# Optimization experiments

Hardware: AMD Instinct MI355X
Metric: run time of the kernel (lower is better)

## Reference

```python
import jax, jax.numpy as jnp
import numpy as np

B, T, C = 2, 2048, 2048
N_HEAD, N_KV_HEAD, HEAD_DIM = 16, 4, 128
N_REP = N_HEAD // N_KV_HEAD
EPS = 1e-05


def setup_inputs() -> dict:
    key = jax.random.key(0)
    ks = jax.random.split(key, 8)
    # rope freqs as cos/sin of theta_t,i = t / 10000^(2i/d)
    inv_freq = 1.0 / (10000.0 ** (np.arange(0, HEAD_DIM, 2, dtype=np.float32) / HEAD_DIM))
    ang = np.arange(T, dtype=np.float32)[:, None] * inv_freq[None, :]  # [T, HEAD_DIM//2]
    scale = 0.02
    return {
        "x": jax.random.normal(ks[0], (B, T, C), jnp.float32),
        "freqs_cos": jnp.asarray(np.cos(ang)),
        "freqs_sin": jnp.asarray(np.sin(ang)),
        "wq": jax.random.normal(ks[1], (C, N_HEAD * HEAD_DIM), jnp.float32) * scale,
        "wk": jax.random.normal(ks[2], (C, N_KV_HEAD * HEAD_DIM), jnp.float32) * scale,
        "wv": jax.random.normal(ks[3], (C, N_KV_HEAD * HEAD_DIM), jnp.float32) * scale,
        "wo": jax.random.normal(ks[4], (N_HEAD * HEAD_DIM, C), jnp.float32) * scale,
        "q_norm_w": jnp.ones((HEAD_DIM,), jnp.float32),
        "k_norm_w": jnp.ones((HEAD_DIM,), jnp.float32),
    }


def _rmsnorm(x, w):
    var = jnp.mean(jnp.square(x), axis=-1, keepdims=True)
    return x * jax.lax.rsqrt(var + EPS) * w


def _rope(x, cos, sin):
    # x: [B, T, H, D]; interpret last dim as interleaved (real, imag) pairs
    xr = x[..., 0::2]
    xi = x[..., 1::2]
    c = cos[None, :, None, :]
    s = sin[None, :, None, :]
    out_r = xr * c - xi * s
    out_i = xr * s + xi * c
    return jnp.stack([out_r, out_i], axis=-1).reshape(x.shape)


def reference(x, freqs_cos, freqs_sin, wq, wk, wv, wo, q_norm_w, k_norm_w):
    # QKV projections
    xq = (x @ wq).reshape(B, T, N_HEAD, HEAD_DIM)
    xk = (x @ wk).reshape(B, T, N_KV_HEAD, HEAD_DIM)
    xv = (x @ wv).reshape(B, T, N_KV_HEAD, HEAD_DIM)
    # optional q/k RMSNorm (use_qk_norm=True)
    xq = _rmsnorm(xq, q_norm_w)
    xk = _rmsnorm(xk, k_norm_w)
    # RoPE
    xq = _rope(xq, freqs_cos, freqs_sin)
    xk = _rope(xk, freqs_cos, freqs_sin)
    # GQA expand: each kv head repeated N_REP times contiguously
    xk = jnp.repeat(xk, N_REP, axis=2)  # [B, T, N_HEAD, D]
    xv = jnp.repeat(xv, N_REP, axis=2)
    # causal SDPA
    scores = jnp.einsum("bthd,bshd->bhts", xq, xk) / jnp.sqrt(jnp.float32(HEAD_DIM))
    causal = jnp.tril(jnp.ones((T, T), bool))
    scores = jnp.where(causal[None, None], scores, jnp.float32(-1e30))
    attn = jax.nn.softmax(scores, axis=-1)
    y = jnp.einsum("bhts,bshd->bthd", attn, xv).reshape(B, T, N_HEAD * HEAD_DIM)
    return y @ wo
```

## Files before the change

### kernel.cpp

```cpp
#include <hip/hip_runtime.h>
#include <hip/hip_bf16.h>

using u16 = unsigned short;
using u32 = unsigned int;

typedef short bf16x8 __attribute__((ext_vector_type(8)));
typedef float f32x4 __attribute__((ext_vector_type(4)));

#define AS1 __attribute__((address_space(1)))
#define AS3 __attribute__((address_space(3)))

__device__ __forceinline__ void gll16(const void* g, void* l) {
  __builtin_amdgcn_global_load_lds((const AS1 u32*)g, (AS3 u32*)l, 16, 0, 0);
}

__device__ __forceinline__ u16 f2bf(float x) {
  u32 u = __builtin_bit_cast(u32, x);
  u32 r = (u + 0x7fffu + ((u >> 16) & 1u)) >> 16;
  return (u16)r;
}
__device__ __forceinline__ u32 pk2(float lo, float hi) {
  return (u32)f2bf(lo) | ((u32)f2bf(hi) << 16);
}
__device__ __forceinline__ u16 f2bf_fast(float x) {
  __hip_bfloat16 h = __float2bfloat16(x);
  return __builtin_bit_cast(u16, h);
}

__device__ __forceinline__ void trans64(const float* __restrict__ in, u16* __restrict__ out,
                                        int R, int Cc, int bx, int by, float (*tl)[65]) {
  int c0 = bx * 64, r0 = by * 64, tid = threadIdx.x;
#pragma unroll
  for (int i = 0; i < 16; i++) {
    int idx = i * 256 + tid; int tr = idx >> 6, tc = idx & 63;
    tl[tr][tc] = in[(size_t)(r0 + tr) * Cc + c0 + tc];
  }
  __syncthreads();
#pragma unroll
  for (int i = 0; i < 16; i++) {
    int idx = i * 256 + tid; int tr = idx >> 6, tc = idx & 63;
    out[(size_t)(c0 + tr) * R + r0 + tc] = f2bf(tl[tc][tr]);
  }
}

__global__ void k_prep(const float* __restrict__ x, u16* __restrict__ xb,
                       const float* __restrict__ wq, u16* __restrict__ wqt,
                       const float* __restrict__ wk, const float* __restrict__ wv,
                       u16* __restrict__ wkvt,
                       const float* __restrict__ wo, u16* __restrict__ wot,
                       const float* __restrict__ fc, const float* __restrict__ fs,
                       float2* __restrict__ fcs) {
  __shared__ float tl[64][65];
  int gid = blockIdx.x;
  if (gid < 4096) {
    int i = gid * 256 + threadIdx.x;
    const float4* p = (const float4*)(x + (size_t)i * 8);
    float4 a = p[0], b = p[1];
    uint4 o;
    o.x = pk2(a.x, a.y); o.y = pk2(a.z, a.w);
    o.z = pk2(b.x, b.y); o.w = pk2(b.z, b.w);
    *(uint4*)(xb + (size_t)i * 8) = o;
  } else if (gid < 5120) {
    int t = gid - 4096; trans64(wq, wqt, 2048, 2048, t & 31, t >> 5, tl);
  } else if (gid < 5376) {
    int t = gid - 5120; trans64(wk, wkvt, 2048, 512, t & 7, t >> 3, tl);
  } else if (gid < 5632) {
    int t = gid - 5376; trans64(wv, wkvt + 512 * 2048, 2048, 512, t & 7, t >> 3, tl);
  } else if (gid < 6656) {
    int t = gid - 5632; trans64(wo, wot, 2048, 2048, t & 31, t >> 5, tl);
  } else {
    int base = (gid - 6656) * 2048 + threadIdx.x * 8;
#pragma unroll
    for (int j = 0; j < 8; j++) {
      int idx = base + j;
      fcs[idx] = make_float2(fc[idx], fs[idx]);
    }
  }
}

__global__ __launch_bounds__(512, 2) void k_gemm_qkv(
    const u16* __restrict__ A, const u16* __restrict__ BT0, const u16* __restrict__ BT1,
    u16* __restrict__ Qout, u16* __restrict__ Kout, u16* __restrict__ Vout,
    const float* __restrict__ nwq, const float* __restrict__ nwk,
    const float2* __restrict__ fcs) {
  __shared__ char lds[131072];
  const int K = 2048;
  int tid = threadIdx.x, w = tid >> 6, l = tid & 63, lg = l >> 4, ll = l & 15;
  int wr = w >> 2, wc = w & 3;
  int lid = blockIdx.y * 24 + blockIdx.x;
  int xcd = lid & 7, r = lid >> 3;
  int colg = xcd & 1, rowg = xcd >> 1;
  int bxt = colg * 12 + r % 12;
  int bm0 = (rowg * 8 + r / 12) * 128;
  bool qpath = (bxt < 16);
  const u16* BT = qpath ? BT0 : BT1;
  int bn0 = qpath ? bxt * 128 : (bxt - 16) * 128;

  auto stage = [&](int si, int kt) {
    char* Sb = lds + si * 32768;
    int k0 = kt * 64;
#pragma unroll
    for (int i = 0; i < 2; i++) {
      int base = i * 512 + (w << 6);
      int c = base + l;
      int row = c >> 3, kc = (c & 7) ^ (row & 7);
      gll16(A + (size_t)(bm0 + row) * K + k0 + kc * 8, Sb + base * 16);
      gll16(BT + (size_t)(bn0 + row) * K + k0 + kc * 8, Sb + 16384 + base * 16);
    }
  };

  f32x4 acc[4][2] = {};
  stage(0, 0); stage(1, 1); stage(2, 2);
  asm volatile("s_waitcnt vmcnt(8)" ::: "memory");
  __builtin_amdgcn_s_barrier();
  __builtin_amdgcn_sched_barrier(0);

  for (int kt = 0; kt < 32; ++kt) {
    int cs = kt & 3;
    if (kt + 3 < 32) stage((kt + 3) & 3, kt + 3);
    char* As = lds + cs * 32768;
    char* Bs = As + 16384;
    __builtin_amdgcn_s_setprio(1);
#pragma unroll
    for (int ks = 0; ks < 2; ks++) {
      bf16x8 af[4], bf[2];
#pragma unroll
      for (int m = 0; m < 4; m++) {
        int row = 64 * wr + 16 * m + ll;
        af[m] = *(const bf16x8*)(As + row * 128 + (((lg + 4 * ks) ^ (row & 7)) << 4));
      }
#pragma unroll
      for (int n = 0; n < 2; n++) {
        int row = 32 * wc + 16 * n + ll;
        bf[n] = *(const bf16x8*)(Bs + row * 128 + (((lg + 4 * ks) ^ (row & 7)) << 4));
      }
#pragma unroll
      for (int m = 0; m < 4; m++)
#pragma unroll
        for (int n = 0; n < 2; n++)
          acc[m][n] = __builtin_amdgcn_mfma_f32_16x16x32_bf16(af[m], bf[n], acc[m][n], 0, 0, 0);
    }
    __builtin_amdgcn_s_setprio(0);
    if (kt <= 28) {
      asm volatile("s_waitcnt vmcnt(8)" ::: "memory");
    } else if (kt == 29) {
      asm volatile("s_waitcnt vmcnt(4)" ::: "memory");
    } else {
      asm volatile("s_waitcnt vmcnt(0)" ::: "memory");
    }
    __builtin_amdgcn_s_barrier();
    __builtin_amdgcn_sched_barrier(0);
  }

  if (qpath || bn0 < 512) {
    const float* nw = qpath ? nwq : nwk;
    u16* O = qpath ? Qout : Kout;
    int ostride = qpath ? 2048 : 512;
    float outscale = qpath ? 0.12751744843f : 1.0f;
    float* ssum = (float*)lds;
    float ps[4][4];
#pragma unroll
    for (int m = 0; m < 4; m++)
#pragma unroll
      for (int r2 = 0; r2 < 4; r2++) {
        float p = 0.f;
#pragma unroll
        for (int n = 0; n < 2; n++) p += acc[m][n][r2] * acc[m][n][r2];
#pragma unroll
        for (int msk = 1; msk < 16; msk <<= 1) p += __shfl_xor(p, msk);
        ps[m][r2] = p;
      }
    if (ll == 0) {
#pragma unroll
      for (int m = 0; m < 4; m++)
#pragma unroll
        for (int r2 = 0; r2 < 4; r2++)
          ssum[wr * 256 + (16 * m + 4 * lg + r2) * 4 + wc] = ps[m][r2];
    }
    __syncthreads();
    float rs[4][4];
#pragma unroll
    for (int m = 0; m < 4; m++)
#pragma unroll
      for (int r2 = 0; r2 < 4; r2++) {
        int rowl = 16 * m + 4 * lg + r2;
        const float* sp = ssum + wr * 256 + rowl * 4;
        float tot = sp[0] + sp[1] + sp[2] + sp[3];
        rs[m][r2] = rsqrtf(tot * (1.0f / 128.0f) + 1e-5f) * outscale;
      }
#pragma unroll
    for (int m = 0; m < 4; m++)
#pragma unroll
      for (int n = 0; n < 2; n++) {
        int col = bn0 + 32 * wc + 16 * n + ll;
        int d = col & 127;
        float wgt = nw[d];
        int i = d >> 1;
#pragma unroll
        for (int r2 = 0; r2 < 4; r2++) {
          int row = bm0 + 64 * wr + 16 * m + 4 * lg + r2;
          int t = row & 2047;
          float y = acc[m][n][r2] * rs[m][r2] * wgt;
          float p = __shfl_xor(y, 1);
          float2 cs2 = fcs[t * 64 + i];
          float o = (ll & 1) ? (p * cs2.y + y * cs2.x) : (y * cs2.x - p * cs2.y);
          O[(size_t)row * ostride + col] = f2bf(o);
        }
      }
  } else {
    int b = bm0 >> 11, t0g = bm0 & 2047;
    int kvh = (bn0 - 512) >> 7;
    int bk = b * 4 + kvh;
#pragma unroll
    for (int m = 0; m < 4; m++)
#pragma unroll
      for (int n = 0; n < 2; n++) {
        int d = 32 * wc + 16 * n + ll;
        int tloc = 64 * wr + 16 * m + 4 * lg;
        u32 w0 = pk2(acc[m][n][0], acc[m][n][1]);
        u32 w1 = pk2(acc[m][n][2], acc[m][n][3]);
        int byte = (d * 256 + tloc * 2) ^ ((d & 7) << 4);
        *(uint2*)(lds + byte) = make_uint2(w0, w1);
      }
    __syncthreads();
    int tc = tid & 15, dbase = tid >> 4;
#pragma unroll
    for (int pass = 0; pass < 4; pass++) {
      int d = dbase + pass * 32;
      int byte = (d * 256 + tc * 16) ^ ((d & 7) << 4);
      uint4 v = *(const uint4*)(lds + byte);
      *(uint4*)(Vout + ((size_t)(bk * 128 + d)) * 2048 + t0g + tc * 8) = v;
    }
  }
}

__global__ __launch_bounds__(512, 2) void k_gemm_o(
    const u16* __restrict__ A, const u16* __restrict__ BT, float* __restrict__ C) {
  __shared__ char lds[131072];
  const int K = 2048;
  int tid = threadIdx.x, w = tid >> 6, l = tid & 63, lg = l >> 4, ll = l & 15;
  int wr = w >> 2, wc = w & 3;
  int lid = blockIdx.y * 16 + blockIdx.x;
  int xcd = lid & 7, r = lid >> 3;
  int colg = xcd & 1, rowg = xcd >> 1;
  int bxt = colg * 8 + r % 8;
  int bm0 = (rowg * 8 + r / 8) * 128;
  int bn0 = bxt * 128;

  auto stage = [&](int si, int kt) {
    char* Sb = lds + si * 32768;
    int k0 = kt * 64;
#pragma unroll
    for (int i = 0; i < 2; i++) {
      int base = i * 512 + (w << 6);
      int c = base + l;
      int row = c >> 3, kc = (c & 7) ^ (row & 7);
      gll16(A + (size_t)(bm0 + row) * K + k0 + kc * 8, Sb + base * 16);
      gll16(BT + (size_t)(bn0 + row) * K + k0 + kc * 8, Sb + 16384 + base * 16);
    }
  };

  f32x4 acc[4][2] = {};
  stage(0, 0); stage(1, 1); stage(2, 2);
  asm volatile("s_waitcnt vmcnt(8)" ::: "memory");
  __builtin_amdgcn_s_barrier();
  __builtin_amdgcn_sched_barrier(0);

  for (int kt = 0; kt < 32; ++kt) {
    int cs = kt & 3;
    if (kt + 3 < 32) stage((kt + 3) & 3, kt + 3);
    char* As = lds + cs * 32768;
    char* Bs = As + 16384;
    __builtin_amdgcn_s_setprio(1);
#pragma unroll
    for (int ks = 0; ks < 2; ks++) {
      bf16x8 af[4], bf[2];
#pragma unroll
      for (int m = 0; m < 4; m++) {
        int row = 64 * wr + 16 * m + ll;
        af[m] = *(const bf16x8*)(As + row * 128 + (((lg + 4 * ks) ^ (row & 7)) << 4));
      }
#pragma unroll
      for (int n = 0; n < 2; n++) {
        int row = 32 * wc + 16 * n + ll;
        bf[n] = *(const bf16x8*)(Bs + row * 128 + (((lg + 4 * ks) ^ (row & 7)) << 4));
      }
#pragma unroll
      for (int m = 0; m < 4; m++)
#pragma unroll
        for (int n = 0; n < 2; n++)
          acc[m][n] = __builtin_amdgcn_mfma_f32_16x16x32_bf16(af[m], bf[n], acc[m][n], 0, 0, 0);
    }
    __builtin_amdgcn_s_setprio(0);
    if (kt <= 28) {
      asm volatile("s_waitcnt vmcnt(8)" ::: "memory");
    } else if (kt == 29) {
      asm volatile("s_waitcnt vmcnt(4)" ::: "memory");
    } else {
      asm volatile("s_waitcnt vmcnt(0)" ::: "memory");
    }
    __builtin_amdgcn_s_barrier();
    __builtin_amdgcn_sched_barrier(0);
  }

#pragma unroll
  for (int m = 0; m < 4; m++)
#pragma unroll
    for (int n = 0; n < 2; n++) {
      int row = bm0 + 64 * wr + 16 * m + 4 * lg;
      int col = bn0 + 32 * wc + 16 * n + ll;
      float* cp = C + (size_t)row * 2048 + col;
#pragma unroll
      for (int r2 = 0; r2 < 4; r2++) cp[(size_t)r2 * 2048] = acc[m][n][r2];
    }
}

__global__ __launch_bounds__(256, 4) void k_attn(
    const u16* __restrict__ Q, const u16* __restrict__ Kb,
    const u16* __restrict__ Vt, u16* __restrict__ Y) {
  __shared__ char lds[73728];
  char* Ps = lds + 65536;
  int tid = threadIdx.x, w = tid >> 6, l = tid & 63, lg = l >> 4, ll = l & 15;
  int fid = blockIdx.x;
  int g = fid & 7, rank = fid >> 3;
  int b = g >> 2, kvh = g & 3;
  int h = kvh * 4 + (rank & 3);
  int pairId = rank >> 2;
  const u16* Kbase = Kb + ((size_t)b * 2048) * 512 + kvh * 128;
  const u16* Vbase = Vt + ((size_t)(b * 4 + kvh) * 128) * 2048;

  const bf16x8 vones = {(short)0x3F80, (short)0x3F80, (short)0x3F80, (short)0x3F80,
                        (short)0x3F80, (short)0x3F80, (short)0x3F80, (short)0x3F80};

#pragma unroll 1
  for (int qi = 0; qi < 2; qi++) {
    int qb = qi ? (31 - pairId) : pairId;
    int q0 = qb * 64;
    bf16x8 qf[4];
    {
      int qrow = b * 2048 + q0 + 16 * w + ll;
      const u16* qp = Q + (size_t)qrow * 2048 + h * 128;
#pragma unroll
      for (int ks = 0; ks < 4; ks++) qf[ks] = *(const bf16x8*)(qp + ks * 32 + lg * 8);
    }
    f32x4 o[8] = {};
    f32x4 lacc = {};

    auto stage = [&](int bi, int k0) {
      char* Kd = lds + (bi ? 32768 : 0);
      char* Vd = lds + (bi ? 49152 : 16384);
#pragma unroll
      for (int i = 0; i < 4; i++) {
        int c = i * 256 + tid;
        int dst = (i * 256 + (w << 6)) * 16;
        int krow = c >> 4, ksrc = (c & 15) ^ (krow & 7);
        gll16(Kbase + (size_t)(k0 + krow) * 512 + ksrc * 8, Kd + dst);
        int vd = c >> 3, vsrc = (c & 7) ^ (vd & 7);
        gll16(Vbase + (size_t)vd * 2048 + k0 + vsrc * 8, Vd + dst);
      }
    };

    stage(0, 0);
    asm volatile("s_waitcnt vmcnt(0)" ::: "memory");
    __syncthreads();

    int cur = 0;
    for (int it = 0; it <= qb; ++it) {
      if (it < qb) stage(cur ^ 1, (it + 1) * 64);
      char* Ks = lds + (cur ? 32768 : 0);
      char* Vs = lds + (cur ? 49152 : 16384);
      f32x4 s[4] = {};
      __builtin_amdgcn_s_setprio(1);
#pragma unroll
      for (int ks = 0; ks < 4; ks++) {
#pragma unroll
        for (int n = 0; n < 4; n++) {
          int row = 16 * n + ll;
          bf16x8 kf = *(const bf16x8*)(Ks + ((row * 256 + (lg + 4 * ks) * 16) ^ ((row & 7) << 4)));
          s[n] = __builtin_amdgcn_mfma_f32_16x16x32_bf16(qf[ks], kf, s[n], 0, 0, 0);
        }
      }
      __builtin_amdgcn_s_setprio(0);
      if (it == qb) {
        int k0 = it * 64;
#pragma unroll
        for (int n = 0; n < 4; n++) {
          int kk = k0 + 16 * n + ll;
#pragma unroll
          for (int r = 0; r < 4; r++) {
            int qq = q0 + 16 * w + 4 * lg + r;
            if (kk > qq) s[n][r] = -1e30f;
          }
        }
      }
#pragma unroll
      for (int r = 0; r < 4; r++) {
        int prow = 4 * lg + r;
#pragma unroll
        for (int n = 0; n < 4; n++) {
          float e = exp2f(s[n][r]);
          int byte = (w << 11) + ((prow * 128 + (16 * n + ll) * 2) ^ ((prow & 7) << 4));
          *(u16*)(Ps + byte) = f2bf_fast(e);
        }
      }
      __builtin_amdgcn_s_setprio(1);
#pragma unroll
      for (int ks = 0; ks < 2; ks++) {
        bf16x8 pf = *(const bf16x8*)(Ps + (w << 11) + ((ll * 128 + (lg + 4 * ks) * 16) ^ ((ll & 7) << 4)));
        lacc = __builtin_amdgcn_mfma_f32_16x16x32_bf16(pf, vones, lacc, 0, 0, 0);
#pragma unroll
        for (int n = 0; n < 8; n++) {
          int row = 16 * n + ll;
          bf16x8 vf = *(const bf16x8*)(Vs + ((row * 128 + (lg + 4 * ks) * 16) ^ ((row & 7) << 4)));
          o[n] = __builtin_amdgcn_mfma_f32_16x16x32_bf16(pf, vf, o[n], 0, 0, 0);
        }
      }
      __builtin_amdgcn_s_setprio(0);
      asm volatile("s_waitcnt vmcnt(0)" ::: "memory");
      __syncthreads();
      cur ^= 1;
    }
    float rl[4];
#pragma unroll
    for (int r = 0; r < 4; r++) rl[r] = 1.0f / lacc[r];
#pragma unroll
    for (int n = 0; n < 8; n++) {
      int col = h * 128 + 16 * n + ll;
#pragma unroll
      for (int r = 0; r < 4; r++) {
        int trow = b * 2048 + q0 + 16 * w + 4 * lg + r;
        Y[(size_t)trow * 2048 + col] = f2bf_fast(o[n][r] * rl[r]);
      }
    }
  }
  (void)Vbase;
}

extern "C" void kernel_launch(void* const* d_in, const int* in_sizes, int n_in,
                              void* d_out, int out_size, void* d_ws, size_t ws_size,
                              hipStream_t stream) {
  const float* x   = (const float*)d_in[0];
  const float* fc  = (const float*)d_in[1];
  const float* fs  = (const float*)d_in[2];
  const float* wq  = (const float*)d_in[3];
  const float* wk  = (const float*)d_in[4];
  const float* wv  = (const float*)d_in[5];
  const float* wo  = (const float*)d_in[6];
  const float* qnw = (const float*)d_in[7];
  const float* knw = (const float*)d_in[8];
  float* out = (float*)d_out;

  const size_t MB = 1ull << 20;
  char* ws = (char*)d_ws;
  u16*    xb   = (u16*)(ws);
  u16*    wqt  = (u16*)(ws + 16 * MB);
  u16*    wkvt = (u16*)(ws + 24 * MB);
  u16*    wot  = (u16*)(ws + 28 * MB);
  u16*    Qb   = (u16*)(ws + 36 * MB);
  u16*    Kbq  = (u16*)(ws + 52 * MB);
  u16*    Vtg  = (u16*)(ws + 56 * MB);
  u16*    Yb   = (u16*)(ws + 60 * MB);
  float2* fcs  = (float2*)(ws + 76 * MB);

  hipLaunchKernelGGL(k_prep, dim3(6720), dim3(256), 0, stream,
                     x, xb, wq, wqt, wk, wv, wkvt, wo, wot, fc, fs, fcs);
  hipLaunchKernelGGL(k_gemm_qkv, dim3(24, 32), dim3(512), 0, stream,
                     xb, wqt, wkvt, Qb, Kbq, Vtg, qnw, knw, fcs);
  hipLaunchKernelGGL(k_attn, dim3(512), dim3(256), 0, stream, Qb, Kbq, Vtg, Yb);
  hipLaunchKernelGGL(k_gemm_o, dim3(16, 32), dim3(512), 0, stream, Yb, wot, out);
}
```

Before: 204.7 us.

## Share K/V tiles across the four GQA query heads in one attention block

The attention kernel now runs 512-thread blocks in which the 8 waves cover the 4 query heads of one KV head times two 16-row groups of a 32-row query tile. Each K/V tile staged into LDS is therefore reused by all heads in the GQA group, where before each block loaded it for a single head. The aim is to cut redundant global/L2 traffic for K and V and halve the grid size. The cost is more LDS per block (P scratch grows), smaller query tiles, which add causal-boundary waste and make the last tile's mask cover a 64-wide key tile, and lower block occupancy.

```diff
diff --git a/kernel.cpp b/kernel.cpp
--- a/kernel.cpp
+++ b/kernel.cpp
@@ -315,60 +315,62 @@
     }
 }
 
-__global__ __launch_bounds__(256, 4) void k_attn(
+__global__ __launch_bounds__(512, 2) void k_attn(
     const u16* __restrict__ Q, const u16* __restrict__ Kb,
     const u16* __restrict__ Vt, u16* __restrict__ Y) {
-  __shared__ char lds[73728];
+  __shared__ char lds[81920];
   char* Ps = lds + 65536;
   int tid = threadIdx.x, w = tid >> 6, l = tid & 63, lg = l >> 4, ll = l & 15;
   int fid = blockIdx.x;
   int g = fid & 7, rank = fid >> 3;
   int b = g >> 2, kvh = g & 3;
-  int h = kvh * 4 + (rank & 3);
-  int pairId = rank >> 2;
+  int h = kvh * 4 + (w & 3);
+  int rgrp = w >> 2;
   const u16* Kbase = Kb + ((size_t)b * 2048) * 512 + kvh * 128;
   const u16* Vbase = Vt + ((size_t)(b * 4 + kvh) * 128) * 2048;
 
   const bf16x8 vones = {(short)0x3F80, (short)0x3F80, (short)0x3F80, (short)0x3F80,
                         (short)0x3F80, (short)0x3F80, (short)0x3F80, (short)0x3F80};
 
+  auto stage = [&](int bi, int k0) {
+    char* Kd = lds + (bi ? 32768 : 0);
+    char* Vd = Kd + 16384;
+#pragma unroll
+    for (int i = 0; i < 2; i++) {
+      int base = i * 512 + (w << 6);
+      int c = base + l;
+      int dst = base * 16;
+      int krow = c >> 4, ksrc = (c & 15) ^ (krow & 7);
+      gll16(Kbase + (size_t)(k0 + krow) * 512 + ksrc * 8, Kd + dst);
+      int vd = c >> 3, vsrc = (c & 7) ^ (vd & 7);
+      gll16(Vbase + (size_t)vd * 2048 + k0 + vsrc * 8, Vd + dst);
+    }
+  };
+
 #pragma unroll 1
   for (int qi = 0; qi < 2; qi++) {
-    int qb = qi ? (31 - pairId) : pairId;
-    int q0 = qb * 64;
+    int qt = qi ? (63 - rank) : rank;
+    int q0 = qt * 32;
+    int nt = (qt >> 1) + 1;
     bf16x8 qf[4];
     {
-      int qrow = b * 2048 + q0 + 16 * w + ll;
+      int qrow = b * 2048 + q0 + rgrp * 16 + ll;
       const u16* qp = Q + (size_t)qrow * 2048 + h * 128;
 #pragma unroll
       for (int ks = 0; ks < 4; ks++) qf[ks] = *(const bf16x8*)(qp + ks * 32 + lg * 8);
     }
     f32x4 o[8] = {};
     f32x4 lacc = {};
-
-    auto stage = [&](int bi, int k0) {
-      char* Kd = lds + (bi ? 32768 : 0);
-      char* Vd = lds + (bi ? 49152 : 16384);
-#pragma unroll
-      for (int i = 0; i < 4; i++) {
-        int c = i * 256 + tid;
-        int dst = (i * 256 + (w << 6)) * 16;
-        int krow = c >> 4, ksrc = (c & 15) ^ (krow & 7);
-        gll16(Kbase + (size_t)(k0 + krow) * 512 + ksrc * 8, Kd + dst);
-        int vd = c >> 3, vsrc = (c & 7) ^ (vd & 7);
-        gll16(Vbase + (size_t)vd * 2048 + k0 + vsrc * 8, Vd + dst);
-      }
-    };
 
     stage(0, 0);
     asm volatile("s_waitcnt vmcnt(0)" ::: "memory");
     __syncthreads();
 
     int cur = 0;
-    for (int it = 0; it <= qb; ++it) {
-      if (it < qb) stage(cur ^ 1, (it + 1) * 64);
+    for (int it = 0; it < nt; ++it) {
+      if (it + 1 < nt) stage(cur ^ 1, (it + 1) * 64);
       char* Ks = lds + (cur ? 32768 : 0);
-      char* Vs = lds + (cur ? 49152 : 16384);
+      char* Vs = Ks + 16384;
       f32x4 s[4] = {};
       __builtin_amdgcn_s_setprio(1);
 #pragma unroll
@@ -381,14 +383,14 @@
         }
       }
       __builtin_amdgcn_s_setprio(0);
-      if (it == qb) {
+      if (it == nt - 1) {
         int k0 = it * 64;
 #pragma unroll
         for (int n = 0; n < 4; n++) {
           int kk = k0 + 16 * n + ll;
 #pragma unroll
           for (int r = 0; r < 4; r++) {
-            int qq = q0 + 16 * w + 4 * lg + r;
+            int qq = q0 + rgrp * 16 + 4 * lg + r;
             if (kk > qq) s[n][r] = -1e30f;
           }
         }
@@ -428,12 +430,11 @@
       int col = h * 128 + 16 * n + ll;
 #pragma unroll
       for (int r = 0; r < 4; r++) {
-        int trow = b * 2048 + q0 + 16 * w + 4 * lg + r;
+        int trow = b * 2048 + q0 + rgrp * 16 + 4 * lg + r;
         Y[(size_t)trow * 2048 + col] = f2bf_fast(o[n][r] * rl[r]);
       }
     }
   }
-  (void)Vbase;
 }
 
 extern "C" void kernel_launch(void* const* d_in, const int* in_sizes, int n_in,
@@ -466,6 +467,6 @@
                      x, xb, wq, wqt, wk, wv, wkvt, wo, wot, fc, fs, fcs);
   hipLaunchKernelGGL(k_gemm_qkv, dim3(24, 32), dim3(512), 0, stream,
                      xb, wqt, wkvt, Qb, Kbq, Vtg, qnw, knw, fcs);
-  hipLaunchKernelGGL(k_attn, dim3(512), dim3(256), 0, stream, Qb, Kbq, Vtg, Yb);
+  hipLaunchKernelGGL(k_attn, dim3(256), dim3(512), 0, stream, Qb, Kbq, Vtg, Yb);
   hipLaunchKernelGGL(k_gemm_o, dim3(16, 32), dim3(512), 0, stream, Yb, wot, out);
 }
```

Result: faster. 200.0 us (-2.3%).
